# Kernel optimization log

Hardware: AMD Instinct MI355X
Metric: run time of the kernel (lower is better)

The kernel has to match this reference:

```python
import jax, jax.numpy as jnp
import numpy as np

N_NODES = 100000
N_EDGES = 1600000
IN_C, HID_C, OUT_C = 128, 128, 64


def setup_inputs() -> dict:
    key = jax.random.key(0)
    k1, k2, k3, k4 = jax.random.split(key, 4)
    x = jax.random.normal(k1, (N_NODES, IN_C), dtype=jnp.float32)
    edge_index = jax.random.randint(k2, (2, N_EDGES), 0, N_NODES, dtype=jnp.int32)
    # Glorot-style init scale for the linear weights (matches PyG GCNConv default)
    W1 = jax.random.normal(k3, (IN_C, HID_C), dtype=jnp.float32) * (1.0 / np.sqrt(IN_C))
    b1 = jnp.zeros((HID_C,), dtype=jnp.float32)
    W2 = jax.random.normal(k4, (HID_C, OUT_C), dtype=jnp.float32) * (1.0 / np.sqrt(HID_C))
    b2 = jnp.zeros((OUT_C,), dtype=jnp.float32)
    return {"x": x, "edge_index": edge_index, "W1": W1, "b1": b1, "W2": W2, "b2": b2}


def _gcn_norm(edge_index, num_nodes):
    """Add self-loops and compute symmetric normalization deg^-1/2[src]*deg^-1/2[dst]."""
    src, dst = edge_index[0], edge_index[1]
    loop = jnp.arange(num_nodes, dtype=src.dtype)
    src_f = jnp.concatenate([src, loop])
    dst_f = jnp.concatenate([dst, loop])
    ones = jnp.ones_like(dst_f, dtype=jnp.float32)
    deg = jax.ops.segment_sum(ones, dst_f, num_segments=num_nodes)  # in-degree incl. self-loop
    deg_inv_sqrt = jnp.where(deg > 0, jax.lax.rsqrt(deg), 0.0)
    norm = deg_inv_sqrt[src_f] * deg_inv_sqrt[dst_f]  # [E+N]
    return src_f, dst_f, norm


def _gcn_conv(x, W, b, src_f, dst_f, norm, num_nodes):
    h = x @ W                              # [N, C_out] linear transform first
    msg = h[src_f] * norm[:, None]         # gather + scale, [E+N, C_out]
    agg = jax.ops.segment_sum(msg, dst_f, num_segments=num_nodes)  # scatter-add
    return agg + b


def reference(x, edge_index, W1, b1, W2, b2):
    n = x.shape[0]
    src_f, dst_f, norm = _gcn_norm(edge_index, n)
    h = jax.nn.relu(_gcn_conv(x, W1, b1, src_f, dst_f, norm, n))
    out = _gcn_conv(h, W2, b2, src_f, dst_f, norm, n)
    return out
```

## Files before the change

### kernel.cpp

```cpp
#include <hip/hip_runtime.h>


constexpr int BLK = 256;
constexpr int PCAP = 2560;
constexpr int CPAD = 16;
constexpr int CHUNK = 6144;
constexpr int NBMAX = 800;


__global__ __launch_bounds__(256)
void bucket_sort_kernel(const int* __restrict__ src, const int* __restrict__ dst,
                        int* __restrict__ bcnt, unsigned* __restrict__ ebuf,
                        int e, int nbuck) {
    __shared__ unsigned stage[CHUNK];
    __shared__ unsigned short keys[CHUNK];
    __shared__ int hist[NBMAX];
    __shared__ int excl[NBMAX];
    __shared__ int gbase[NBMAX];
    __shared__ int wsum[256];

    const int t = threadIdx.x;
    const int base = blockIdx.x * CHUNK;
    const int cnt = min(CHUNK, e - base);

    for (int i = t; i < nbuck; i += 256) hist[i] = 0;
    __syncthreads();

    for (int i = t; i < cnt; i += 256) atomicAdd(&hist[dst[base + i] >> 7], 1);
    __syncthreads();

    const int b0 = t * 4;
    int s0 = 0, s1 = 0, s2 = 0, s3 = 0;
    if (b0 < nbuck)     s0 = hist[b0];
    if (b0 + 1 < nbuck) s1 = hist[b0 + 1];
    if (b0 + 2 < nbuck) s2 = hist[b0 + 2];
    if (b0 + 3 < nbuck) s3 = hist[b0 + 3];
    wsum[t] = s0 + s1 + s2 + s3;
    __syncthreads();
    for (int off = 1; off < 256; off <<= 1) {
        int v = (t >= off) ? wsum[t - off] : 0;
        __syncthreads();
        wsum[t] += v;
        __syncthreads();
    }
    int run = (t > 0) ? wsum[t - 1] : 0;
    if (b0 < nbuck)     { excl[b0]     = run; hist[b0]     = run; run += s0; }
    if (b0 + 1 < nbuck) { excl[b0 + 1] = run; hist[b0 + 1] = run; run += s1; }
    if (b0 + 2 < nbuck) { excl[b0 + 2] = run; hist[b0 + 2] = run; run += s2; }
    if (b0 + 3 < nbuck) { excl[b0 + 3] = run; hist[b0 + 3] = run; run += s3; }
    __syncthreads();

    for (int i = t; i < cnt; i += 256) {
        int s = src[base + i], d = dst[base + i];
        int bb = d >> 7;
        int p = atomicAdd(&hist[bb], 1);
        stage[p] = ((unsigned)s << 7) | (unsigned)(d & 127);
        keys[p] = (unsigned short)bb;
    }
    __syncthreads();

    if (b0 < nbuck)     { int c = hist[b0]     - excl[b0];     gbase[b0]     = c ? atomicAdd(&bcnt[b0 * CPAD], c)       : 0; }
    if (b0 + 1 < nbuck) { int c = hist[b0 + 1] - excl[b0 + 1]; gbase[b0 + 1] = c ? atomicAdd(&bcnt[(b0 + 1) * CPAD], c) : 0; }
    if (b0 + 2 < nbuck) { int c = hist[b0 + 2] - excl[b0 + 2]; gbase[b0 + 2] = c ? atomicAdd(&bcnt[(b0 + 2) * CPAD], c) : 0; }
    if (b0 + 3 < nbuck) { int c = hist[b0 + 3] - excl[b0 + 3]; gbase[b0 + 3] = c ? atomicAdd(&bcnt[(b0 + 3) * CPAD], c) : 0; }
    __syncthreads();

    for (int i = t; i < cnt; i += 256) {
        int bb = keys[i];
        int p = gbase[bb] + (i - excl[bb]);
        if (p < PCAP) ebuf[(size_t)bb * PCAP + p] = stage[i];
    }
}


__global__ __launch_bounds__(256)
void build_kernel(const unsigned* __restrict__ ebuf, const int* __restrict__ bcnt,
                  float* __restrict__ dis, int2* __restrict__ rp,
                  int* __restrict__ esrc, int n) {
    __shared__ int packed[PCAP];
    __shared__ int stage[PCAP];
    __shared__ int hist[128];
    __shared__ int excl[128];
    __shared__ int cur[128];

    const int b = blockIdx.x, t = threadIdx.x;
    const int base = b << 7;
    const int nloc = min(128, n - base);
    const int tot = min(bcnt[b * CPAD], PCAP);

    if (t < 128) hist[t] = 0;
    __syncthreads();

    const unsigned* eb = ebuf + (size_t)b * PCAP;
    for (int i = t; i < tot; i += 256) {
        int v = (int)eb[i];
        packed[i] = v;
        atomicAdd(&hist[v & 127], 1);
    }
    __syncthreads();

    if (t < 128) excl[t] = hist[t];
    __syncthreads();
    for (int off = 1; off < 128; off <<= 1) {
        int v = (t >= off && t < 128) ? excl[t - off] : 0;
        __syncthreads();
        if (t < 128) excl[t] += v;
        __syncthreads();
    }

    if (t < 128) {
        int deg = hist[t];
        int start = excl[t] - deg;
        cur[t] = start;
        if (t < nloc) {
            dis[base + t] = rsqrtf((float)(deg + 1));
            int gs = b * PCAP + start;
            rp[base + t] = make_int2(gs, gs + deg);
        }
    }
    __syncthreads();

    for (int i = t; i < tot; i += 256) {
        int v = packed[i];
        int p = atomicAdd(&cur[v & 127], 1);
        stage[p] = v >> 7;
    }
    __syncthreads();

    for (int i = t; i < tot; i += 256) esrc[b * PCAP + i] = stage[i];
}


__device__ __forceinline__ unsigned short f2bf(float f) {
    unsigned u = __float_as_uint(f);
    u += 0x7fffu + ((u >> 16) & 1u);
    return (unsigned short)(u >> 16);
}
__device__ __forceinline__ float bflo(unsigned u) { return __uint_as_float(u << 16); }
__device__ __forceinline__ float bfhi(unsigned u) { return __uint_as_float(u & 0xffff0000u); }
__device__ __forceinline__ unsigned pk2(short a, short b) {
    return (unsigned)(unsigned short)a | ((unsigned)(unsigned short)b << 16);
}

__device__ __forceinline__ void split2(float v, short& hi, short& lo) {
    unsigned short h = f2bf(v);
    float hf = __uint_as_float(((unsigned)h) << 16);
    hi = (short)h;
    lo = (short)f2bf(v - hf);
}

typedef __attribute__((ext_vector_type(8))) short bf16x8;
typedef __attribute__((ext_vector_type(4))) float f32x4;
#define MFMA_B16(a, b, c) __builtin_amdgcn_mfma_f32_16x16x32_bf16(a, b, c, 0, 0, 0)

__device__ __forceinline__ void split8(const float4& a, const float4& b, bf16x8& h, bf16x8& l) {
    short hh, ll;
    split2(a.x, hh, ll); h[0] = hh; l[0] = ll;
    split2(a.y, hh, ll); h[1] = hh; l[1] = ll;
    split2(a.z, hh, ll); h[2] = hh; l[2] = ll;
    split2(a.w, hh, ll); h[3] = hh; l[3] = ll;
    split2(b.x, hh, ll); h[4] = hh; l[4] = ll;
    split2(b.y, hh, ll); h[5] = hh; l[5] = ll;
    split2(b.z, hh, ll); h[6] = hh; l[6] = ll;
    split2(b.w, hh, ll); h[7] = hh; l[7] = ll;
}


__global__ void prep_b_kernel(const float* __restrict__ W1, const float* __restrict__ W2,
                              unsigned short* __restrict__ B1h, unsigned short* __restrict__ B1l,
                              unsigned short* __restrict__ B2h, unsigned short* __restrict__ B2l) {
    const int c = blockIdx.x;
    const int k = threadIdx.x;
    short h, l;
    if (c < 128) {
        split2(W1[(size_t)k * 128 + c], h, l);
        B1h[c * 128 + k] = (unsigned short)h;
        B1l[c * 128 + k] = (unsigned short)l;
    } else {
        const int c2 = c - 128;
        split2(W2[(size_t)k * 64 + c2], h, l);
        B2h[c2 * 128 + k] = (unsigned short)h;
        B2l[c2 * 128 + k] = (unsigned short)l;
    }
}


constexpr int BAS = 72;

__global__ __launch_bounds__(256, 4)
void gemm_mfma(const float* __restrict__ Af,
               const unsigned short* __restrict__ Bh, const unsigned short* __restrict__ Bl,
               const float* __restrict__ dis, unsigned* __restrict__ Cb, int nrows) {
    constexpr int COLS = 128;
    constexpr int CT = COLS / 16;
    constexpr int BE = COLS * BAS;
    constexpr int CSC = COLS + 8;
    constexpr int SMEM = (2 * BE * 2 > 128 * CSC * 2) ? 2 * BE * 2 : 128 * CSC * 2;

    __shared__ __align__(16) char smem[SMEM];
    short* sBh = (short*)smem;
    short* sBl = sBh + BE;

    const int t = threadIdx.x;
    const int rowbase = blockIdx.x * 128;
    const int wave = t >> 6;
    const int lane = t & 63;
    const int quad = lane >> 4;
    const int l16 = lane & 15;

    const int gr0 = rowbase + wave * 32 + l16;
    const int gr1 = gr0 + 16;

    f32x4 acc[2][CT];
#pragma unroll
    for (int rt = 0; rt < 2; ++rt)
#pragma unroll
        for (int ct = 0; ct < CT; ++ct) {
            f32x4 z = {0.f, 0.f, 0.f, 0.f};
            acc[rt][ct] = z;
        }

    for (int half = 0; half < 2; ++half) {
        {
            constexpr int NV = COLS * 8;
            uint4* dh = (uint4*)sBh;
            uint4* dl = (uint4*)sBl;
            const uint4* gh = (const uint4*)Bh;
            const uint4* gl = (const uint4*)Bl;
            for (int idx = t; idx < NV; idx += 256) {
                int c = idx >> 3, kq = idx & 7;
                int gidx = c * 16 + half * 8 + kq;
                int didx = c * 9 + kq;
                dh[didx] = gh[gidx];
                dl[didx] = gl[gidx];
            }
        }
        __syncthreads();

#pragma unroll
        for (int kc = 0; kc < 2; ++kc) {
            const int ko = kc * 32 + quad * 8;
            bf16x8 ah0, al0, ah1, al1;
            float4 va = {0.f, 0.f, 0.f, 0.f}, vb = va, vc = va, vd = va;
            if (gr0 < nrows) {
                const float4* ap = (const float4*)(Af + (size_t)gr0 * 128 + half * 64 + ko);
                va = ap[0]; vb = ap[1];
            }
            if (gr1 < nrows) {
                const float4* ap = (const float4*)(Af + (size_t)gr1 * 128 + half * 64 + ko);
                vc = ap[0]; vd = ap[1];
            }
            split8(va, vb, ah0, al0);
            split8(vc, vd, ah1, al1);
#pragma unroll
            for (int ct = 0; ct < CT; ++ct) {
                const int bo = (ct * 16 + l16) * BAS + ko;
                bf16x8 bh = *(const bf16x8*)&sBh[bo];
                bf16x8 bl = *(const bf16x8*)&sBl[bo];
                acc[0][ct] = MFMA_B16(ah0, bh, acc[0][ct]);
                acc[1][ct] = MFMA_B16(ah1, bh, acc[1][ct]);
                acc[0][ct] = MFMA_B16(al0, bh, acc[0][ct]);
                acc[1][ct] = MFMA_B16(al1, bh, acc[1][ct]);
                acc[0][ct] = MFMA_B16(ah0, bl, acc[0][ct]);
                acc[1][ct] = MFMA_B16(ah1, bl, acc[1][ct]);
            }
        }
        __syncthreads();
    }

    short* Cs = (short*)smem;
    float sv[2][4];
#pragma unroll
    for (int rt = 0; rt < 2; ++rt)
#pragma unroll
        for (int r = 0; r < 4; ++r) {
            int rr = rowbase + wave * 32 + rt * 16 + quad * 4 + r;
            sv[rt][r] = (rr < nrows) ? dis[rr] : 0.f;
        }
#pragma unroll
    for (int rt = 0; rt < 2; ++rt)
#pragma unroll
        for (int ct = 0; ct < CT; ++ct) {
            const int rb = wave * 32 + rt * 16 + quad * 4;
            const int c = ct * 16 + l16;
#pragma unroll
            for (int r = 0; r < 4; ++r)
                Cs[(rb + r) * CSC + c] = (short)f2bf(sv[rt][r] * acc[rt][ct][r]);
        }
    __syncthreads();

    {
        const int row = t >> 1, hf = t & 1;
        const int gr = rowbase + row;
        if (gr < nrows) {
            const uint4* cr = (const uint4*)&Cs[row * CSC + hf * (COLS / 2)];
            uint4* dstp = (uint4*)Cb + (size_t)gr * (COLS / 8) + hf * (COLS / 16);
#pragma unroll
            for (int i = 0; i < COLS / 16; ++i) dstp[i] = cr[i];
        }
    }
}


#define ACCLO(v)                                          \
    acc[0] += bflo(v.x); acc[1] += bfhi(v.x);             \
    acc[2] += bflo(v.y); acc[3] += bfhi(v.y);             \
    acc[4] += bflo(v.z); acc[5] += bfhi(v.z);             \
    acc[6] += bflo(v.w); acc[7] += bfhi(v.w);
#define ACCHI(v)                                          \
    acc[8]  += bflo(v.x); acc[9]  += bfhi(v.x);           \
    acc[10] += bflo(v.y); acc[11] += bfhi(v.y);           \
    acc[12] += bflo(v.z); acc[13] += bfhi(v.z);           \
    acc[14] += bflo(v.w); acc[15] += bfhi(v.w);

__global__ __launch_bounds__(256)
void gather_gemm_kernel(const int2* __restrict__ rp, const int* __restrict__ esrc,
                        const float* __restrict__ dis, const unsigned* __restrict__ hs,
                        const float* __restrict__ bias,
                        const unsigned short* __restrict__ B2h,
                        const unsigned short* __restrict__ B2l,
                        unsigned* __restrict__ h2b, int n) {
    constexpr int ASTR = 136;
    constexpr int CSTR = 72;
    __shared__ __align__(16) short sAh[32 * ASTR];
    __shared__ __align__(16) short sAl[32 * ASTR];

    const int t = threadIdx.x;
    const int base = blockIdx.x * 32;

    {
        const int nl = t >> 3;
        const int l8 = t & 7;
        const int node = base + nl;
        if (node < n) {
            const uint4* h4 = (const uint4*)hs;
            const int2 se = rp[node];
            float acc[16];
            {
                uint4 v0 = h4[(size_t)node * 16 + l8];
                uint4 v1 = h4[(size_t)node * 16 + 8 + l8];
                acc[0] = bflo(v0.x); acc[1] = bfhi(v0.x);
                acc[2] = bflo(v0.y); acc[3] = bfhi(v0.y);
                acc[4] = bflo(v0.z); acc[5] = bfhi(v0.z);
                acc[6] = bflo(v0.w); acc[7] = bfhi(v0.w);
                acc[8]  = bflo(v1.x); acc[9]  = bfhi(v1.x);
                acc[10] = bflo(v1.y); acc[11] = bfhi(v1.y);
                acc[12] = bflo(v1.z); acc[13] = bfhi(v1.z);
                acc[14] = bflo(v1.w); acc[15] = bfhi(v1.w);
            }
            int k = se.x;
            const int end = se.y;
            for (; k + 3 < end; k += 4) {
                int s0 = esrc[k], s1 = esrc[k + 1], s2 = esrc[k + 2], s3 = esrc[k + 3];
                uint4 a0 = h4[(size_t)s0 * 16 + l8], b0 = h4[(size_t)s0 * 16 + 8 + l8];
                uint4 a1 = h4[(size_t)s1 * 16 + l8], b1 = h4[(size_t)s1 * 16 + 8 + l8];
                uint4 a2 = h4[(size_t)s2 * 16 + l8], b2 = h4[(size_t)s2 * 16 + 8 + l8];
                uint4 a3 = h4[(size_t)s3 * 16 + l8], b3 = h4[(size_t)s3 * 16 + 8 + l8];
                ACCLO(a0) ACCHI(b0) ACCLO(a1) ACCHI(b1)
                ACCLO(a2) ACCHI(b2) ACCLO(a3) ACCHI(b3)
            }
            for (; k < end; ++k) {
                int s = esrc[k];
                uint4 a = h4[(size_t)s * 16 + l8], b = h4[(size_t)s * 16 + 8 + l8];
                ACCLO(a) ACCHI(b)
            }

            const float di = dis[node];
            const float4* b4 = (const float4*)bias;
            float4 ba = b4[l8 * 2], bb = b4[l8 * 2 + 1];
            float4 bc = b4[16 + l8 * 2], bd = b4[17 + l8 * 2];
            float v[16];
            v[0]  = fmaxf(fmaf(di, acc[0],  ba.x), 0.f);
            v[1]  = fmaxf(fmaf(di, acc[1],  ba.y), 0.f);
            v[2]  = fmaxf(fmaf(di, acc[2],  ba.z), 0.f);
            v[3]  = fmaxf(fmaf(di, acc[3],  ba.w), 0.f);
            v[4]  = fmaxf(fmaf(di, acc[4],  bb.x), 0.f);
            v[5]  = fmaxf(fmaf(di, acc[5],  bb.y), 0.f);
            v[6]  = fmaxf(fmaf(di, acc[6],  bb.z), 0.f);
            v[7]  = fmaxf(fmaf(di, acc[7],  bb.w), 0.f);
            v[8]  = fmaxf(fmaf(di, acc[8],  bc.x), 0.f);
            v[9]  = fmaxf(fmaf(di, acc[9],  bc.y), 0.f);
            v[10] = fmaxf(fmaf(di, acc[10], bc.z), 0.f);
            v[11] = fmaxf(fmaf(di, acc[11], bc.w), 0.f);
            v[12] = fmaxf(fmaf(di, acc[12], bd.x), 0.f);
            v[13] = fmaxf(fmaf(di, acc[13], bd.y), 0.f);
            v[14] = fmaxf(fmaf(di, acc[14], bd.z), 0.f);
            v[15] = fmaxf(fmaf(di, acc[15], bd.w), 0.f);

            short h0, l0, h1, l1, h2, l2, h3, l3, h4v, l4, h5, l5, h6, l6, h7, l7;
            uint4 oh, ol;
            split2(v[0], h0, l0); split2(v[1], h1, l1); split2(v[2], h2, l2); split2(v[3], h3, l3);
            split2(v[4], h4v, l4); split2(v[5], h5, l5); split2(v[6], h6, l6); split2(v[7], h7, l7);
            oh.x = pk2(h0, h1); oh.y = pk2(h2, h3); oh.z = pk2(h4v, h5); oh.w = pk2(h6, h7);
            ol.x = pk2(l0, l1); ol.y = pk2(l2, l3); ol.z = pk2(l4, l5);  ol.w = pk2(l6, l7);
            *(uint4*)&sAh[nl * ASTR + l8 * 8] = oh;
            *(uint4*)&sAl[nl * ASTR + l8 * 8] = ol;
            split2(v[8], h0, l0); split2(v[9], h1, l1); split2(v[10], h2, l2); split2(v[11], h3, l3);
            split2(v[12], h4v, l4); split2(v[13], h5, l5); split2(v[14], h6, l6); split2(v[15], h7, l7);
            oh.x = pk2(h0, h1); oh.y = pk2(h2, h3); oh.z = pk2(h4v, h5); oh.w = pk2(h6, h7);
            ol.x = pk2(l0, l1); ol.y = pk2(l2, l3); ol.z = pk2(l4, l5);  ol.w = pk2(l6, l7);
            *(uint4*)&sAh[nl * ASTR + 64 + l8 * 8] = oh;
            *(uint4*)&sAl[nl * ASTR + 64 + l8 * 8] = ol;
        } else {
            uint4 z = {0u, 0u, 0u, 0u};
            *(uint4*)&sAh[nl * ASTR + l8 * 8] = z;
            *(uint4*)&sAl[nl * ASTR + l8 * 8] = z;
            *(uint4*)&sAh[nl * ASTR + 64 + l8 * 8] = z;
            *(uint4*)&sAl[nl * ASTR + 64 + l8 * 8] = z;
        }
    }
    __syncthreads();

    const int wave = t >> 6, lane = t & 63, quad = lane >> 4, l16 = lane & 15;
    const int col = wave * 16 + l16;
    f32x4 c0 = {0.f, 0.f, 0.f, 0.f}, c1 = c0;
#pragma unroll
    for (int ks = 0; ks < 4; ++ks) {
        const int ko = ks * 32 + quad * 8;
        bf16x8 bh = *(const bf16x8*)&B2h[col * 128 + ko];
        bf16x8 bl = *(const bf16x8*)&B2l[col * 128 + ko];
        bf16x8 ah0 = *(const bf16x8*)&sAh[l16 * ASTR + ko];
        bf16x8 al0 = *(const bf16x8*)&sAl[l16 * ASTR + ko];
        bf16x8 ah1 = *(const bf16x8*)&sAh[(16 + l16) * ASTR + ko];
        bf16x8 al1 = *(const bf16x8*)&sAl[(16 + l16) * ASTR + ko];
        c0 = MFMA_B16(ah0, bh, c0);
        c1 = MFMA_B16(ah1, bh, c1);
        c0 = MFMA_B16(al0, bh, c0);
        c1 = MFMA_B16(al1, bh, c1);
        c0 = MFMA_B16(ah0, bl, c0);
        c1 = MFMA_B16(ah1, bl, c1);
    }
    __syncthreads();

    short* Cs = sAh;
#pragma unroll
    for (int r = 0; r < 4; ++r) {
        const int row0 = quad * 4 + r, row1 = 16 + quad * 4 + r;
        const float d0 = (base + row0 < n) ? dis[base + row0] : 0.f;
        const float d1 = (base + row1 < n) ? dis[base + row1] : 0.f;
        Cs[row0 * CSTR + col] = (short)f2bf(d0 * c0[r]);
        Cs[row1 * CSTR + col] = (short)f2bf(d1 * c1[r]);
    }
    __syncthreads();
    {
        const int row = t >> 3, l8 = t & 7;
        const int gr = base + row;
        if (gr < n)
            ((uint4*)h2b)[(size_t)gr * 8 + l8] = *(const uint4*)&Cs[row * CSTR + l8 * 8];
    }
}


__global__ __launch_bounds__(256)
void gather_out_kernel(const int2* __restrict__ rp, const int* __restrict__ esrc,
                       const float* __restrict__ dis, const unsigned* __restrict__ hs,
                       const float* __restrict__ bias, float* __restrict__ out, int n) {
    const int gid = blockIdx.x * BLK + threadIdx.x;
    const int node = gid >> 2;
    const int l4 = gid & 3;
    if (node >= n) return;

    const uint4* h4 = (const uint4*)hs;
    const int2 se = rp[node];

    float acc[16];
    {
        uint4 v0 = h4[(size_t)node * 8 + l4];
        uint4 v1 = h4[(size_t)node * 8 + 4 + l4];
        acc[0] = bflo(v0.x); acc[1] = bfhi(v0.x);
        acc[2] = bflo(v0.y); acc[3] = bfhi(v0.y);
        acc[4] = bflo(v0.z); acc[5] = bfhi(v0.z);
        acc[6] = bflo(v0.w); acc[7] = bfhi(v0.w);
        acc[8]  = bflo(v1.x); acc[9]  = bfhi(v1.x);
        acc[10] = bflo(v1.y); acc[11] = bfhi(v1.y);
        acc[12] = bflo(v1.z); acc[13] = bfhi(v1.z);
        acc[14] = bflo(v1.w); acc[15] = bfhi(v1.w);
    }

    int k = se.x;
    const int end = se.y;
    for (; k + 3 < end; k += 4) {
        int s0 = esrc[k], s1 = esrc[k + 1], s2 = esrc[k + 2], s3 = esrc[k + 3];
        uint4 a0 = h4[(size_t)s0 * 8 + l4], b0 = h4[(size_t)s0 * 8 + 4 + l4];
        uint4 a1 = h4[(size_t)s1 * 8 + l4], b1 = h4[(size_t)s1 * 8 + 4 + l4];
        uint4 a2 = h4[(size_t)s2 * 8 + l4], b2 = h4[(size_t)s2 * 8 + 4 + l4];
        uint4 a3 = h4[(size_t)s3 * 8 + l4], b3 = h4[(size_t)s3 * 8 + 4 + l4];
        ACCLO(a0) ACCHI(b0) ACCLO(a1) ACCHI(b1)
        ACCLO(a2) ACCHI(b2) ACCLO(a3) ACCHI(b3)
    }
    for (; k < end; ++k) {
        int s = esrc[k];
        uint4 a = h4[(size_t)s * 8 + l4], b = h4[(size_t)s * 8 + 4 + l4];
        ACCLO(a) ACCHI(b)
    }

    const float di = dis[node];
    const float4* b4 = (const float4*)bias;
    const float4 ba = b4[l4 * 2], bb = b4[l4 * 2 + 1];
    const float4 bc = b4[8 + l4 * 2], bd = b4[9 + l4 * 2];
    float4 o0, o1, o2, o3;
    o0.x = fmaf(di, acc[0],  ba.x); o0.y = fmaf(di, acc[1],  ba.y);
    o0.z = fmaf(di, acc[2],  ba.z); o0.w = fmaf(di, acc[3],  ba.w);
    o1.x = fmaf(di, acc[4],  bb.x); o1.y = fmaf(di, acc[5],  bb.y);
    o1.z = fmaf(di, acc[6],  bb.z); o1.w = fmaf(di, acc[7],  bb.w);
    o2.x = fmaf(di, acc[8],  bc.x); o2.y = fmaf(di, acc[9],  bc.y);
    o2.z = fmaf(di, acc[10], bc.z); o2.w = fmaf(di, acc[11], bc.w);
    o3.x = fmaf(di, acc[12], bd.x); o3.y = fmaf(di, acc[13], bd.y);
    o3.z = fmaf(di, acc[14], bd.z); o3.w = fmaf(di, acc[15], bd.w);
    float4* o4 = (float4*)out;
    o4[(size_t)node * 16 + l4 * 2]     = o0;
    o4[(size_t)node * 16 + l4 * 2 + 1] = o1;
    o4[(size_t)node * 16 + 8 + l4 * 2]     = o2;
    o4[(size_t)node * 16 + 8 + l4 * 2 + 1] = o3;
}

#undef ACCLO
#undef ACCHI


extern "C" void kernel_launch(void* const* d_in, const int* in_sizes, int n_in,
                              void* d_out, int out_size, void* d_ws, size_t ws_size,
                              hipStream_t stream) {
    const float* x  = (const float*)d_in[0];
    const int*   ei = (const int*)d_in[1];
    const float* W1 = (const float*)d_in[2];
    const float* b1 = (const float*)d_in[3];
    const float* W2 = (const float*)d_in[4];
    const float* b2 = (const float*)d_in[5];
    float* out = (float*)d_out;

    const int n = in_sizes[0] / 128;
    const int e = in_sizes[1] / 2;
    const int* src = ei;
    const int* dst = ei + e;

    char* ws = (char*)d_ws;
    float*    dis  = (float*)   (ws + 0x0);
    int2*     rp   = (int2*)    (ws + 0x80000);
    int*      bcnt = (int*)     (ws + 0x180000);
    unsigned short* B1h = (unsigned short*)(ws + 0x1A0000);
    unsigned short* B1l = (unsigned short*)(ws + 0x1A8000);
    unsigned short* B2h = (unsigned short*)(ws + 0x1B0000);
    unsigned short* B2l = (unsigned short*)(ws + 0x1B4000);
    int*      esrc = (int*)     (ws + 0x280000);
    unsigned* hb   = (unsigned*)(ws + 0xB00000);
    unsigned* h2b  = (unsigned*)(ws + 0x2400000);
    unsigned* ebuf = (unsigned*)(ws + 0x2400000);

    const int nbuck = (n + 127) >> 7;
    const int nb_g = (n + 127) / 128;

    hipMemsetAsync(bcnt, 0, (size_t)nbuck * CPAD * 4, stream);
    prep_b_kernel<<<192, 128, 0, stream>>>(W1, W2, B1h, B1l, B2h, B2l);
    bucket_sort_kernel<<<(e + CHUNK - 1) / CHUNK, 256, 0, stream>>>(src, dst, bcnt, ebuf, e, nbuck);
    build_kernel<<<nbuck, 256, 0, stream>>>(ebuf, bcnt, dis, rp, esrc, n);

    gemm_mfma<<<nb_g, 256, 0, stream>>>(x, B1h, B1l, dis, hb, n);

    gather_gemm_kernel<<<(n + 31) / 32, 256, 0, stream>>>(
        rp, esrc, dis, hb, b1, B2h, B2l, h2b, n);

    gather_out_kernel<<<(n * 4 + BLK - 1) / BLK, BLK, 0, stream>>>(
        rp, esrc, dis, h2b, b2, out, n);
}
```

Before: 266.4 us.

## Sort nodes by degree and widen gather lanes per node in aggregation kernels

Builds a degree histogram in the CSR build, scans it and computes a permutation of nodes grouped by in-degree. Both gather kernels then process nodes in that order, so wavefronts hold nodes of similar degree and lose less time to lane divergence. The first gather kernel also moves to 512 threads with 16 lanes per node, each loading one uint4, instead of 8 lanes loading two; only half the threads run the MFMA stage. The cost is two extra small kernels, a global atomic histogram, scattered output writes through the permutation, and worse locality for the self-row and output accesses.

```diff
diff --git a/kernel.cpp b/kernel.cpp
--- a/kernel.cpp
+++ b/kernel.cpp
@@ -76,7 +76,7 @@
 __global__ __launch_bounds__(256)
 void build_kernel(const unsigned* __restrict__ ebuf, const int* __restrict__ bcnt,
                   float* __restrict__ dis, int2* __restrict__ rp,
-                  int* __restrict__ esrc, int n) {
+                  int* __restrict__ esrc, int* __restrict__ deghist, int n) {
     __shared__ int packed[PCAP];
     __shared__ int stage[PCAP];
     __shared__ int hist[128];
@@ -116,6 +116,7 @@
             dis[base + t] = rsqrtf((float)(deg + 1));
             int gs = b * PCAP + start;
             rp[base + t] = make_int2(gs, gs + deg);
+            atomicAdd(&deghist[min(deg, 255)], 1);
         }
     }
     __syncthreads();
@@ -128,6 +129,31 @@
     __syncthreads();
 
     for (int i = t; i < tot; i += 256) esrc[b * PCAP + i] = stage[i];
+}
+
+
+__global__ void deg_scan_kernel(const int* __restrict__ deghist, int* __restrict__ cursor) {
+    __shared__ int s[256];
+    const int t = threadIdx.x;
+    s[t] = deghist[t];
+    __syncthreads();
+    for (int off = 1; off < 256; off <<= 1) {
+        int v = (t >= off) ? s[t - off] : 0;
+        __syncthreads();
+        s[t] += v;
+        __syncthreads();
+    }
+    cursor[t] = (t > 0) ? s[t - 1] : 0;
+}
+
+__global__ void perm_kernel(const int2* __restrict__ rp, int* __restrict__ cursor,
+                            int* __restrict__ perm, int n) {
+    const int i = blockIdx.x * 256 + threadIdx.x;
+    if (i >= n) return;
+    const int2 se = rp[i];
+    const int deg = min(se.y - se.x, 255);
+    const int pos = atomicAdd(&cursor[deg], 1);
+    perm[pos] = i;
 }
 
 
@@ -302,6 +328,135 @@
 }
 
 
+#define ACC8(v)                                           \
+    acc[0] += bflo(v.x); acc[1] += bfhi(v.x);             \
+    acc[2] += bflo(v.y); acc[3] += bfhi(v.y);             \
+    acc[4] += bflo(v.z); acc[5] += bfhi(v.z);             \
+    acc[6] += bflo(v.w); acc[7] += bfhi(v.w);
+
+__global__ __launch_bounds__(512)
+void gather_gemm_kernel(const int* __restrict__ perm,
+                        const int2* __restrict__ rp, const int* __restrict__ esrc,
+                        const float* __restrict__ dis, const unsigned* __restrict__ hs,
+                        const float* __restrict__ bias,
+                        const unsigned short* __restrict__ B2h,
+                        const unsigned short* __restrict__ B2l,
+                        unsigned* __restrict__ h2b, int n) {
+    constexpr int ASTR = 136;
+    constexpr int CSTR = 72;
+    __shared__ __align__(16) short sAh[32 * ASTR];
+    __shared__ __align__(16) short sAl[32 * ASTR];
+    __shared__ int snode[32];
+
+    const int t = threadIdx.x;
+    const int base = blockIdx.x * 32;
+
+    {
+        const int nl = t >> 4;
+        const int lc = t & 15;
+        int node = -1;
+        if (base + nl < n) node = perm[base + nl];
+        if (lc == 0) snode[nl] = node;
+
+        if (node >= 0) {
+            const uint4* h4 = (const uint4*)hs;
+            const int2 se = rp[node];
+            float acc[8];
+            {
+                uint4 v = h4[(size_t)node * 16 + lc];
+                acc[0] = bflo(v.x); acc[1] = bfhi(v.x);
+                acc[2] = bflo(v.y); acc[3] = bfhi(v.y);
+                acc[4] = bflo(v.z); acc[5] = bfhi(v.z);
+                acc[6] = bflo(v.w); acc[7] = bfhi(v.w);
+            }
+            int k = se.x;
+            const int end = se.y;
+            for (; k + 3 < end; k += 4) {
+                int s0 = esrc[k], s1 = esrc[k + 1], s2 = esrc[k + 2], s3 = esrc[k + 3];
+                uint4 v0 = h4[(size_t)s0 * 16 + lc];
+                uint4 v1 = h4[(size_t)s1 * 16 + lc];
+                uint4 v2 = h4[(size_t)s2 * 16 + lc];
+                uint4 v3 = h4[(size_t)s3 * 16 + lc];
+                ACC8(v0) ACC8(v1) ACC8(v2) ACC8(v3)
+            }
+            for (; k < end; ++k) {
+                uint4 v = h4[(size_t)esrc[k] * 16 + lc];
+                ACC8(v)
+            }
+
+            const float di = dis[node];
+            const float4 ba = ((const float4*)bias)[lc * 2];
+            const float4 bb = ((const float4*)bias)[lc * 2 + 1];
+            float v0 = fmaxf(fmaf(di, acc[0], ba.x), 0.f);
+            float v1 = fmaxf(fmaf(di, acc[1], ba.y), 0.f);
+            float v2 = fmaxf(fmaf(di, acc[2], ba.z), 0.f);
+            float v3 = fmaxf(fmaf(di, acc[3], ba.w), 0.f);
+            float v4 = fmaxf(fmaf(di, acc[4], bb.x), 0.f);
+            float v5 = fmaxf(fmaf(di, acc[5], bb.y), 0.f);
+            float v6 = fmaxf(fmaf(di, acc[6], bb.z), 0.f);
+            float v7 = fmaxf(fmaf(di, acc[7], bb.w), 0.f);
+
+            short h0, l0, h1, l1, h2, l2, h3, l3, h4v, l4, h5, l5, h6, l6, h7, l7;
+            split2(v0, h0, l0); split2(v1, h1, l1); split2(v2, h2, l2); split2(v3, h3, l3);
+            split2(v4, h4v, l4); split2(v5, h5, l5); split2(v6, h6, l6); split2(v7, h7, l7);
+            uint4 oh, ol;
+            oh.x = pk2(h0, h1); oh.y = pk2(h2, h3); oh.z = pk2(h4v, h5); oh.w = pk2(h6, h7);
+            ol.x = pk2(l0, l1); ol.y = pk2(l2, l3); ol.z = pk2(l4, l5);  ol.w = pk2(l6, l7);
+            *(uint4*)&sAh[nl * ASTR + lc * 8] = oh;
+            *(uint4*)&sAl[nl * ASTR + lc * 8] = ol;
+        } else {
+            uint4 z = {0u, 0u, 0u, 0u};
+            *(uint4*)&sAh[nl * ASTR + lc * 8] = z;
+            *(uint4*)&sAl[nl * ASTR + lc * 8] = z;
+        }
+    }
+    __syncthreads();
+
+    const int wave = t >> 6, lane = t & 63, quad = lane >> 4, l16 = lane & 15;
+    const int col = wave * 16 + l16;
+    f32x4 c0 = {0.f, 0.f, 0.f, 0.f}, c1 = c0;
+    if (t < 256) {
+#pragma unroll
+        for (int ks = 0; ks < 4; ++ks) {
+            const int ko = ks * 32 + quad * 8;
+            bf16x8 bh = *(const bf16x8*)&B2h[col * 128 + ko];
+            bf16x8 bl = *(const bf16x8*)&B2l[col * 128 + ko];
+            bf16x8 ah0 = *(const bf16x8*)&sAh[l16 * ASTR + ko];
+            bf16x8 al0 = *(const bf16x8*)&sAl[l16 * ASTR + ko];
+            bf16x8 ah1 = *(const bf16x8*)&sAh[(16 + l16) * ASTR + ko];
+            bf16x8 al1 = *(const bf16x8*)&sAl[(16 + l16) * ASTR + ko];
+            c0 = MFMA_B16(ah0, bh, c0);
+            c1 = MFMA_B16(ah1, bh, c1);
+            c0 = MFMA_B16(al0, bh, c0);
+            c1 = MFMA_B16(al1, bh, c1);
+            c0 = MFMA_B16(ah0, bl, c0);
+            c1 = MFMA_B16(ah1, bl, c1);
+        }
+    }
+    __syncthreads();
+
+    short* Cs = sAh;
+    if (t < 256) {
+#pragma unroll
+        for (int r = 0; r < 4; ++r) {
+            const int row0 = quad * 4 + r, row1 = 16 + quad * 4 + r;
+            const int g0 = snode[row0], g1 = snode[row1];
+            const float d0 = (g0 >= 0) ? dis[g0] : 0.f;
+            const float d1 = (g1 >= 0) ? dis[g1] : 0.f;
+            Cs[row0 * CSTR + col] = (short)f2bf(d0 * c0[r]);
+            Cs[row1 * CSTR + col] = (short)f2bf(d1 * c1[r]);
+        }
+    }
+    __syncthreads();
+    if (t < 256) {
+        const int row = t >> 3, l8 = t & 7;
+        const int g = snode[row];
+        if (g >= 0)
+            ((uint4*)h2b)[(size_t)g * 8 + l8] = *(const uint4*)&Cs[row * CSTR + l8 * 8];
+    }
+}
+
+
 #define ACCLO(v)                                          \
     acc[0] += bflo(v.x); acc[1] += bfhi(v.x);             \
     acc[2] += bflo(v.y); acc[3] += bfhi(v.y);             \
@@ -314,151 +469,15 @@
     acc[14] += bflo(v.w); acc[15] += bfhi(v.w);
 
 __global__ __launch_bounds__(256)
-void gather_gemm_kernel(const int2* __restrict__ rp, const int* __restrict__ esrc,
-                        const float* __restrict__ dis, const unsigned* __restrict__ hs,
-                        const float* __restrict__ bias,
-                        const unsigned short* __restrict__ B2h,
-                        const unsigned short* __restrict__ B2l,
-                        unsigned* __restrict__ h2b, int n) {
-    constexpr int ASTR = 136;
-    constexpr int CSTR = 72;
-    __shared__ __align__(16) short sAh[32 * ASTR];
-    __shared__ __align__(16) short sAl[32 * ASTR];
-
-    const int t = threadIdx.x;
-    const int base = blockIdx.x * 32;
-
-    {
-        const int nl = t >> 3;
-        const int l8 = t & 7;
-        const int node = base + nl;
-        if (node < n) {
-            const uint4* h4 = (const uint4*)hs;
-            const int2 se = rp[node];
-            float acc[16];
-            {
-                uint4 v0 = h4[(size_t)node * 16 + l8];
-                uint4 v1 = h4[(size_t)node * 16 + 8 + l8];
-                acc[0] = bflo(v0.x); acc[1] = bfhi(v0.x);
-                acc[2] = bflo(v0.y); acc[3] = bfhi(v0.y);
-                acc[4] = bflo(v0.z); acc[5] = bfhi(v0.z);
-                acc[6] = bflo(v0.w); acc[7] = bfhi(v0.w);
-                acc[8]  = bflo(v1.x); acc[9]  = bfhi(v1.x);
-                acc[10] = bflo(v1.y); acc[11] = bfhi(v1.y);
-                acc[12] = bflo(v1.z); acc[13] = bfhi(v1.z);
-                acc[14] = bflo(v1.w); acc[15] = bfhi(v1.w);
-            }
-            int k = se.x;
-            const int end = se.y;
-            for (; k + 3 < end; k += 4) {
-                int s0 = esrc[k], s1 = esrc[k + 1], s2 = esrc[k + 2], s3 = esrc[k + 3];
-                uint4 a0 = h4[(size_t)s0 * 16 + l8], b0 = h4[(size_t)s0 * 16 + 8 + l8];
-                uint4 a1 = h4[(size_t)s1 * 16 + l8], b1 = h4[(size_t)s1 * 16 + 8 + l8];
-                uint4 a2 = h4[(size_t)s2 * 16 + l8], b2 = h4[(size_t)s2 * 16 + 8 + l8];
-                uint4 a3 = h4[(size_t)s3 * 16 + l8], b3 = h4[(size_t)s3 * 16 + 8 + l8];
-                ACCLO(a0) ACCHI(b0) ACCLO(a1) ACCHI(b1)
-                ACCLO(a2) ACCHI(b2) ACCLO(a3) ACCHI(b3)
-            }
-            for (; k < end; ++k) {
-                int s = esrc[k];
-                uint4 a = h4[(size_t)s * 16 + l8], b = h4[(size_t)s * 16 + 8 + l8];
-                ACCLO(a) ACCHI(b)
-            }
-
-            const float di = dis[node];
-            const float4* b4 = (const float4*)bias;
-            float4 ba = b4[l8 * 2], bb = b4[l8 * 2 + 1];
-            float4 bc = b4[16 + l8 * 2], bd = b4[17 + l8 * 2];
-            float v[16];
-            v[0]  = fmaxf(fmaf(di, acc[0],  ba.x), 0.f);
-            v[1]  = fmaxf(fmaf(di, acc[1],  ba.y), 0.f);
-            v[2]  = fmaxf(fmaf(di, acc[2],  ba.z), 0.f);
-            v[3]  = fmaxf(fmaf(di, acc[3],  ba.w), 0.f);
-            v[4]  = fmaxf(fmaf(di, acc[4],  bb.x), 0.f);
-            v[5]  = fmaxf(fmaf(di, acc[5],  bb.y), 0.f);
-            v[6]  = fmaxf(fmaf(di, acc[6],  bb.z), 0.f);
-            v[7]  = fmaxf(fmaf(di, acc[7],  bb.w), 0.f);
-            v[8]  = fmaxf(fmaf(di, acc[8],  bc.x), 0.f);
-            v[9]  = fmaxf(fmaf(di, acc[9],  bc.y), 0.f);
-            v[10] = fmaxf(fmaf(di, acc[10], bc.z), 0.f);
-            v[11] = fmaxf(fmaf(di, acc[11], bc.w), 0.f);
-            v[12] = fmaxf(fmaf(di, acc[12], bd.x), 0.f);
-            v[13] = fmaxf(fmaf(di, acc[13], bd.y), 0.f);
-            v[14] = fmaxf(fmaf(di, acc[14], bd.z), 0.f);
-            v[15] = fmaxf(fmaf(di, acc[15], bd.w), 0.f);
-
-            short h0, l0, h1, l1, h2, l2, h3, l3, h4v, l4, h5, l5, h6, l6, h7, l7;
-            uint4 oh, ol;
-            split2(v[0], h0, l0); split2(v[1], h1, l1); split2(v[2], h2, l2); split2(v[3], h3, l3);
-            split2(v[4], h4v, l4); split2(v[5], h5, l5); split2(v[6], h6, l6); split2(v[7], h7, l7);
-            oh.x = pk2(h0, h1); oh.y = pk2(h2, h3); oh.z = pk2(h4v, h5); oh.w = pk2(h6, h7);
-            ol.x = pk2(l0, l1); ol.y = pk2(l2, l3); ol.z = pk2(l4, l5);  ol.w = pk2(l6, l7);
-            *(uint4*)&sAh[nl * ASTR + l8 * 8] = oh;
-            *(uint4*)&sAl[nl * ASTR + l8 * 8] = ol;
-            split2(v[8], h0, l0); split2(v[9], h1, l1); split2(v[10], h2, l2); split2(v[11], h3, l3);
-            split2(v[12], h4v, l4); split2(v[13], h5, l5); split2(v[14], h6, l6); split2(v[15], h7, l7);
-            oh.x = pk2(h0, h1); oh.y = pk2(h2, h3); oh.z = pk2(h4v, h5); oh.w = pk2(h6, h7);
-            ol.x = pk2(l0, l1); ol.y = pk2(l2, l3); ol.z = pk2(l4, l5);  ol.w = pk2(l6, l7);
-            *(uint4*)&sAh[nl * ASTR + 64 + l8 * 8] = oh;
-            *(uint4*)&sAl[nl * ASTR + 64 + l8 * 8] = ol;
-        } else {
-            uint4 z = {0u, 0u, 0u, 0u};
-            *(uint4*)&sAh[nl * ASTR + l8 * 8] = z;
-            *(uint4*)&sAl[nl * ASTR + l8 * 8] = z;
-            *(uint4*)&sAh[nl * ASTR + 64 + l8 * 8] = z;
-            *(uint4*)&sAl[nl * ASTR + 64 + l8 * 8] = z;
-        }
-    }
-    __syncthreads();
-
-    const int wave = t >> 6, lane = t & 63, quad = lane >> 4, l16 = lane & 15;
-    const int col = wave * 16 + l16;
-    f32x4 c0 = {0.f, 0.f, 0.f, 0.f}, c1 = c0;
-#pragma unroll
-    for (int ks = 0; ks < 4; ++ks) {
-        const int ko = ks * 32 + quad * 8;
-        bf16x8 bh = *(const bf16x8*)&B2h[col * 128 + ko];
-        bf16x8 bl = *(const bf16x8*)&B2l[col * 128 + ko];
-        bf16x8 ah0 = *(const bf16x8*)&sAh[l16 * ASTR + ko];
-        bf16x8 al0 = *(const bf16x8*)&sAl[l16 * ASTR + ko];
-        bf16x8 ah1 = *(const bf16x8*)&sAh[(16 + l16) * ASTR + ko];
-        bf16x8 al1 = *(const bf16x8*)&sAl[(16 + l16) * ASTR + ko];
-        c0 = MFMA_B16(ah0, bh, c0);
-        c1 = MFMA_B16(ah1, bh, c1);
-        c0 = MFMA_B16(al0, bh, c0);
-        c1 = MFMA_B16(al1, bh, c1);
-        c0 = MFMA_B16(ah0, bl, c0);
-        c1 = MFMA_B16(ah1, bl, c1);
-    }
-    __syncthreads();
-
-    short* Cs = sAh;
-#pragma unroll
-    for (int r = 0; r < 4; ++r) {
-        const int row0 = quad * 4 + r, row1 = 16 + quad * 4 + r;
-        const float d0 = (base + row0 < n) ? dis[base + row0] : 0.f;
-        const float d1 = (base + row1 < n) ? dis[base + row1] : 0.f;
-        Cs[row0 * CSTR + col] = (short)f2bf(d0 * c0[r]);
-        Cs[row1 * CSTR + col] = (short)f2bf(d1 * c1[r]);
-    }
-    __syncthreads();
-    {
-        const int row = t >> 3, l8 = t & 7;
-        const int gr = base + row;
-        if (gr < n)
-            ((uint4*)h2b)[(size_t)gr * 8 + l8] = *(const uint4*)&Cs[row * CSTR + l8 * 8];
-    }
-}
-
-
-__global__ __launch_bounds__(256)
-void gather_out_kernel(const int2* __restrict__ rp, const int* __restrict__ esrc,
+void gather_out_kernel(const int* __restrict__ perm,
+                       const int2* __restrict__ rp, const int* __restrict__ esrc,
                        const float* __restrict__ dis, const unsigned* __restrict__ hs,
                        const float* __restrict__ bias, float* __restrict__ out, int n) {
     const int gid = blockIdx.x * BLK + threadIdx.x;
-    const int node = gid >> 2;
+    const int ni = gid >> 2;
     const int l4 = gid & 3;
-    if (node >= n) return;
+    if (ni >= n) return;
+    const int node = perm[ni];
 
     const uint4* h4 = (const uint4*)hs;
     const int2 se = rp[node];
@@ -514,6 +533,7 @@
     o4[(size_t)node * 16 + 8 + l4 * 2 + 1] = o3;
 }
 
+#undef ACC8
 #undef ACCLO
 #undef ACCHI
 
@@ -538,10 +558,13 @@
     float*    dis  = (float*)   (ws + 0x0);
     int2*     rp   = (int2*)    (ws + 0x80000);
     int*      bcnt = (int*)     (ws + 0x180000);
+    int*      deghist = (int*)  (ws + 0x190000);
+    int*      cursor  = (int*)  (ws + 0x190400);
     unsigned short* B1h = (unsigned short*)(ws + 0x1A0000);
     unsigned short* B1l = (unsigned short*)(ws + 0x1A8000);
     unsigned short* B2h = (unsigned short*)(ws + 0x1B0000);
     unsigned short* B2l = (unsigned short*)(ws + 0x1B4000);
+    int*      perm = (int*)     (ws + 0x1C0000);
     int*      esrc = (int*)     (ws + 0x280000);
     unsigned* hb   = (unsigned*)(ws + 0xB00000);
     unsigned* h2b  = (unsigned*)(ws + 0x2400000);
@@ -550,16 +573,19 @@
     const int nbuck = (n + 127) >> 7;
     const int nb_g = (n + 127) / 128;
 
-    hipMemsetAsync(bcnt, 0, (size_t)nbuck * CPAD * 4, stream);
+    hipMemsetAsync(bcnt, 0, 0x11000, stream);
     prep_b_kernel<<<192, 128, 0, stream>>>(W1, W2, B1h, B1l, B2h, B2l);
     bucket_sort_kernel<<<(e + CHUNK - 1) / CHUNK, 256, 0, stream>>>(src, dst, bcnt, ebuf, e, nbuck);
-    build_kernel<<<nbuck, 256, 0, stream>>>(ebuf, bcnt, dis, rp, esrc, n);
+    build_kernel<<<nbuck, 256, 0, stream>>>(ebuf, bcnt, dis, rp, esrc, deghist, n);
+
+    deg_scan_kernel<<<1, 256, 0, stream>>>(deghist, cursor);
+    perm_kernel<<<(n + 255) / 256, 256, 0, stream>>>(rp, cursor, perm, n);
 
     gemm_mfma<<<nb_g, 256, 0, stream>>>(x, B1h, B1l, dis, hb, n);
 
-    gather_gemm_kernel<<<(n + 31) / 32, 256, 0, stream>>>(
-        rp, esrc, dis, hb, b1, B2h, B2l, h2b, n);
+    gather_gemm_kernel<<<(n + 31) / 32, 512, 0, stream>>>(
+        perm, rp, esrc, dis, hb, b1, B2h, B2l, h2b, n);
 
     gather_out_kernel<<<(n * 4 + BLK - 1) / BLK, BLK, 0, stream>>>(
-        rp, esrc, dis, h2b, b2, out, n);
-}
+        perm, rp, esrc, dis, h2b, b2, out, n);
+}
```

Result: slower. 786.7 us (+195.4%).
